# Optimization experiments

Measured on AMD Instinct MI355X. Metric: run time of the kernel, lower is better.

The kernel has to match this reference:

```python
import jax, jax.numpy as jnp
import numpy as np

NCONF, NT, NX = 8192, 64, 64


def setup_inputs() -> dict:
    key = jax.random.key(0)
    k1, k2, k3 = jax.random.split(key, 3)
    phi = jax.random.normal(k1, (NCONF, NT, NX), dtype=jnp.float32)
    # Well-conditioned invertible mixing matrix so logdet is finite/stable.
    W = jnp.eye(NX, dtype=jnp.float32) + 0.1 * jax.random.normal(k2, (NX, NX), dtype=jnp.float32)
    b = 0.1 * jax.random.normal(k3, (NX,), dtype=jnp.float32)
    return {"phi": phi, "W": W, "b": b}


def _nn(phi, W, b):
    # Wrapped NN: invertible linear coupling along the Nx axis.
    NNphi = jnp.einsum('btx,xy->bty', phi, W) + b
    _, logabsdet = jnp.linalg.slogdet(W)
    logDet = jnp.full((phi.shape[0],), phi.shape[1] * logabsdet, dtype=phi.dtype)
    return NNphi, logDet


def reference(phi, W, b):
    Nconf, Nt, Nx = phi.shape
    # t[i, x] = argmin over time of |phi[i, :, x]|  -> [Nconf, Nx]
    t = jnp.argmin(jnp.abs(phi), axis=1)
    # Source: if t[i,0] > t[i,1]: T0[i] = t[i,1]; config.flip(1) is DISCARDED (no-op).
    T0 = jnp.where(t[:, 0] > t[:, 1], t[:, 1], t[:, 0])  # [Nconf]
    j = jnp.arange(Nx)
    # torch.roll(x, s, dim): out[j] = x[(j - s) % N]
    idx_fwd = (j[None, :] - T0[:, None]) % Nx          # [Nconf, Nx]
    phi_r = jnp.take_along_axis(phi, idx_fwd[:, None, :], axis=2)
    NNphi, logDet = _nn(phi_r, W, b)
    # roll back with shift -T0; flip again discarded in source.
    idx_bwd = (j[None, :] + T0[:, None]) % Nx
    NNphi = jnp.take_along_axis(NNphi, idx_bwd[:, None, :], axis=2)
    return NNphi, logDet
```

## Files before the change

### kernel.cpp

```cpp
#include <hip/hip_runtime.h>
#include <stdint.h>


typedef _Float16 half2v __attribute__((ext_vector_type(2)));
typedef _Float16 half8v __attribute__((ext_vector_type(8)));
typedef float float4v __attribute__((ext_vector_type(4)));

#if defined(__has_builtin)
#if __has_builtin(__builtin_amdgcn_fdot2)
#define HAVE_FDOT2 1
#endif
#endif

__device__ __forceinline__ float dot2f(half2v a, half2v b, float c) {
#ifdef HAVE_FDOT2
  return __builtin_amdgcn_fdot2(a, b, c, false);
#else
  return c + (float)a.x * (float)b.x + (float)a.y * (float)b.y;
#endif
}

union H8 {
  half8v v;
  half2v p[4];
};

__global__ __launch_bounds__(64) void equiv_kernel(
    const float* __restrict__ phi, const float* __restrict__ W,
    const float* __restrict__ b, float* __restrict__ out) {
  __shared__ float smemF[4096];
  _Float16* sPhi = (_Float16*)smemF;
  _Float16* sW = ((_Float16*)smemF) + 4096;
  const int lane = threadIdx.x;

  if (blockIdx.x == 0) {
    float* A = smemF;
    for (int r = 0; r < 64; ++r) A[r * 64 + lane] = W[r * 64 + lane];
    __syncthreads();
    float ldsum = 0.f;
    for (int k = 0; k < 64; ++k) {
      __syncthreads();
      unsigned long long key = 0ull;
      if (lane >= k) {
        float v = fabsf(A[lane * 64 + k]);
        key = (((unsigned long long)__float_as_uint(v)) << 6) | (unsigned long long)lane;
      }
#pragma unroll
      for (int m = 1; m < 64; m <<= 1) {
        unsigned long long o = __shfl_xor(key, m);
        key = (o > key) ? o : key;
      }
      int p = (int)(key & 63ull);
      if (p != k) {
        float tk = A[k * 64 + lane], tp = A[p * 64 + lane];
        A[k * 64 + lane] = tp;
        A[p * 64 + lane] = tk;
      }
      __syncthreads();
      float akk = A[k * 64 + k];
      ldsum += logf(fabsf(akk));
      float rk = 1.0f / akk;
      float pivrow = A[k * 64 + lane];
      for (int t = k + 1; t < 64; ++t) {
        float m = A[t * 64 + k] * rk;
        if (lane > k) A[t * 64 + lane] -= m * pivrow;
      }
    }
    float ld = 64.0f * ldsum;
    float* outLD = out + (size_t)8192 * 4096;
    for (int it = 0; it < 128; ++it) outLD[it * 64 + lane] = ld;
    return;
  }

  const int cfg = (int)blockIdx.x - 1;
  const float4v* phiv = (const float4v*)(phi + (size_t)cfg * 4096);
  const float4v* Wv = (const float4v*)W;

  float4v pv[16], wv[16];
#pragma unroll
  for (int it = 0; it < 16; ++it) pv[it] = phiv[it * 64 + lane];
#pragma unroll
  for (int it = 0; it < 16; ++it) wv[it] = Wv[it * 64 + lane];

  unsigned long long k0 = ~0ull, k1 = ~0ull;
  if ((lane & 15) == 0) {
#pragma unroll
    for (int it = 0; it < 16; ++it) {
      int t = it * 4 + (lane >> 4);
      unsigned long long c0 =
          (((unsigned long long)__float_as_uint(fabsf(pv[it].x))) << 6) | (unsigned long long)t;
      unsigned long long c1 =
          (((unsigned long long)__float_as_uint(fabsf(pv[it].y))) << 6) | (unsigned long long)t;
      k0 = c0 < k0 ? c0 : k0;
      k1 = c1 < k1 ? c1 : k1;
    }
  }
#pragma unroll
  for (int m = 1; m < 64; m <<= 1) {
    unsigned long long o0 = __shfl_xor(k0, m);
    unsigned long long o1 = __shfl_xor(k1, m);
    k0 = o0 < k0 ? o0 : k0;
    k1 = o1 < k1 ? o1 : k1;
  }
  int t0i = (int)(k0 & 63ull), t1i = (int)(k1 & 63ull);
  int T0 = (t0i > t1i) ? t1i : t0i;

#pragma unroll
  for (int it = 0; it < 16; ++it) {
    int flat4 = it * 64 + lane;
    int t = flat4 >> 4;
    int xg = (flat4 & 15) << 2;
    int tsw = t >> 3;
#pragma unroll
    for (int kk = 0; kk < 4; ++kk) {
      int xp = (xg + kk + T0) & 63;
      int pos = t * 64 + ((((xp >> 3) ^ tsw) << 3) | (xp & 7));
      sPhi[pos] = (_Float16)pv[it][kk];
    }
  }
#pragma unroll
  for (int it = 0; it < 16; ++it) {
    int flat4 = it * 64 + lane;
    int xp = flat4 >> 4;
    int cg = (flat4 & 15) << 2;
#pragma unroll
    for (int kk = 0; kk < 4; ++kk) {
      int j = (cg + kk + 64 - T0) & 63;
      int pos = j * 64 + ((((xp >> 3) ^ (j >> 3)) << 3) | (xp & 7));
      sW[pos] = (_Float16)wv[it][kk];
    }
  }
  __syncthreads();

  const int ty = lane >> 3, tx = lane & 7;
  const int t0 = ty << 3, j0 = tx << 3;
  float acc[8][8];
#pragma unroll
  for (int r = 0; r < 8; ++r)
#pragma unroll
    for (int c = 0; c < 8; ++c) acc[r][c] = 0.f;

  for (int xb = 0; xb < 8; ++xb) {
    H8 a[8];
#pragma unroll
    for (int r = 0; r < 8; ++r)
      a[r].v = *(const half8v*)&sPhi[(t0 + r) * 64 + ((xb ^ ty) << 3)];
#pragma unroll
    for (int c = 0; c < 8; ++c) {
      H8 bb;
      bb.v = *(const half8v*)&sW[(j0 + c) * 64 + ((xb ^ tx) << 3)];
#pragma unroll
      for (int r = 0; r < 8; ++r) {
        float av = acc[r][c];
#pragma unroll
        for (int p = 0; p < 4; ++p) av = dot2f(a[r].p[p], bb.p[p], av);
        acc[r][c] = av;
      }
    }
  }

  float bv[8];
#pragma unroll
  for (int c = 0; c < 8; ++c) bv[c] = b[(j0 + c + T0) & 63];
  float* outp = out + (size_t)cfg * 4096;
#pragma unroll
  for (int r = 0; r < 8; ++r) {
#pragma unroll
    for (int cq = 0; cq < 2; ++cq) {
      float4v o;
#pragma unroll
      for (int kk = 0; kk < 4; ++kk) o[kk] = acc[r][cq * 4 + kk] + bv[cq * 4 + kk];
      *(float4v*)&outp[(t0 + r) * 64 + j0 + (cq << 2)] = o;
    }
  }
}

extern "C" void kernel_launch(void* const* d_in, const int* in_sizes, int n_in,
                              void* d_out, int out_size, void* d_ws, size_t ws_size,
                              hipStream_t stream) {
  const float* phi = (const float*)d_in[0];
  const float* W = (const float*)d_in[1];
  const float* b = (const float*)d_in[2];
  float* out = (float*)d_out;
  equiv_kernel<<<dim3(8193), dim3(64), 0, stream>>>(phi, W, b, out);
}
```

Baseline: 289.7 us.

## Precompute shifted fp16 W copies and pack four configs per block

Rolling phi by T0 is folded into the weights. A prep kernel writes all 64 doubly-shifted fp16 copies of W into workspace, and the main kernel reads the copy for its T0 straight from global memory/cache instead of scattering W into LDS for every configuration. Phi is now stored to LDS unshifted, using vectorized half4 stores. Each 256-thread block handles four configurations, one per wave, and the determinant path drops its barriers and uses a padded LDS layout. In exchange the inner GEMM loop now takes its B operand from global/L1, which may add latency, and there is an extra kernel launch plus a 512KB workspace.

```diff
diff --git a/kernel.cpp b/kernel.cpp
--- a/kernel.cpp
+++ b/kernel.cpp
@@ -3,6 +3,7 @@
 
 
 typedef _Float16 half2v __attribute__((ext_vector_type(2)));
+typedef _Float16 half4v __attribute__((ext_vector_type(4)));
 typedef _Float16 half8v __attribute__((ext_vector_type(8)));
 typedef float float4v __attribute__((ext_vector_type(4)));
 
@@ -25,26 +26,39 @@
   half2v p[4];
 };
 
-__global__ __launch_bounds__(64) void equiv_kernel(
+__global__ __launch_bounds__(256) void wt2_prep(const float* __restrict__ W,
+                                                _Float16* __restrict__ wt2) {
+  const int s = blockIdx.x;
+  const int tid = threadIdx.x;
+#pragma unroll
+  for (int it = 0; it < 16; ++it) {
+    int flat = it * 256 + tid;
+    int j = flat >> 6;
+    int y = flat & 63;
+    float v = W[((y + s) & 63) * 64 + ((j + s) & 63)];
+    wt2[(size_t)s * 4096 + flat] = (_Float16)v;
+  }
+}
+
+__global__ __launch_bounds__(256) void equiv_main(
     const float* __restrict__ phi, const float* __restrict__ W,
-    const float* __restrict__ b, float* __restrict__ out) {
-  __shared__ float smemF[4096];
-  _Float16* sPhi = (_Float16*)smemF;
-  _Float16* sW = ((_Float16*)smemF) + 4096;
-  const int lane = threadIdx.x;
+    const float* __restrict__ b, const _Float16* __restrict__ wt2,
+    float* __restrict__ out) {
+  __shared__ __align__(16) unsigned char smem[32768];
+  const int lane = threadIdx.x & 63;
 
   if (blockIdx.x == 0) {
-    float* A = smemF;
-    for (int r = 0; r < 64; ++r) A[r * 64 + lane] = W[r * 64 + lane];
-    __syncthreads();
+    if (threadIdx.x >= 64) return;
+    float* A = (float*)smem;
+    const int t = lane;
+    for (int r = 0; r < 64; ++r) A[r * 65 + lane] = W[r * 64 + lane];
     float ldsum = 0.f;
     for (int k = 0; k < 64; ++k) {
-      __syncthreads();
-      unsigned long long key = 0ull;
-      if (lane >= k) {
-        float v = fabsf(A[lane * 64 + k]);
-        key = (((unsigned long long)__float_as_uint(v)) << 6) | (unsigned long long)lane;
-      }
+      float av = (t >= k) ? fabsf(A[t * 65 + k]) : -1.0f;
+      unsigned long long key =
+          (((unsigned long long)__float_as_uint(av < 0.f ? 0.f : av)) << 6) |
+          (unsigned long long)t;
+      if (t < k) key = 0ull;
 #pragma unroll
       for (int m = 1; m < 64; m <<= 1) {
         unsigned long long o = __shfl_xor(key, m);
@@ -52,18 +66,18 @@
       }
       int p = (int)(key & 63ull);
       if (p != k) {
-        float tk = A[k * 64 + lane], tp = A[p * 64 + lane];
-        A[k * 64 + lane] = tp;
-        A[p * 64 + lane] = tk;
+        float vk = A[k * 65 + lane];
+        float vp = A[p * 65 + lane];
+        A[k * 65 + lane] = vp;
+        A[p * 65 + lane] = vk;
       }
-      __syncthreads();
-      float akk = A[k * 64 + k];
-      ldsum += logf(fabsf(akk));
-      float rk = 1.0f / akk;
-      float pivrow = A[k * 64 + lane];
-      for (int t = k + 1; t < 64; ++t) {
-        float m = A[t * 64 + k] * rk;
-        if (lane > k) A[t * 64 + lane] -= m * pivrow;
+      float piv = A[k * 65 + k];
+      ldsum += logf(fabsf(piv));
+      float rk = 1.0f / piv;
+      float m = (t > k) ? A[t * 65 + k] * rk : 0.f;
+      for (int c = k + 1; c < 64; ++c) {
+        float pr = A[k * 65 + c];
+        if (t > k) A[t * 65 + c] -= m * pr;
       }
     }
     float ld = 64.0f * ldsum;
@@ -72,25 +86,24 @@
     return;
   }
 
-  const int cfg = (int)blockIdx.x - 1;
+  const int wave = threadIdx.x >> 6;
+  const int cfg = ((int)blockIdx.x - 1) * 4 + wave;
+  _Float16* sPhi = ((_Float16*)smem) + wave * 4096;
+
   const float4v* phiv = (const float4v*)(phi + (size_t)cfg * 4096);
-  const float4v* Wv = (const float4v*)W;
-
-  float4v pv[16], wv[16];
+  float4v pv[16];
 #pragma unroll
   for (int it = 0; it < 16; ++it) pv[it] = phiv[it * 64 + lane];
-#pragma unroll
-  for (int it = 0; it < 16; ++it) wv[it] = Wv[it * 64 + lane];
 
   unsigned long long k0 = ~0ull, k1 = ~0ull;
   if ((lane & 15) == 0) {
 #pragma unroll
     for (int it = 0; it < 16; ++it) {
-      int t = it * 4 + (lane >> 4);
+      int tt = it * 4 + (lane >> 4);
       unsigned long long c0 =
-          (((unsigned long long)__float_as_uint(fabsf(pv[it].x))) << 6) | (unsigned long long)t;
+          (((unsigned long long)__float_as_uint(fabsf(pv[it].x))) << 6) | (unsigned long long)tt;
       unsigned long long c1 =
-          (((unsigned long long)__float_as_uint(fabsf(pv[it].y))) << 6) | (unsigned long long)t;
+          (((unsigned long long)__float_as_uint(fabsf(pv[it].y))) << 6) | (unsigned long long)tt;
       k0 = c0 < k0 ? c0 : k0;
       k1 = c1 < k1 ? c1 : k1;
     }
@@ -103,37 +116,26 @@
     k1 = o1 < k1 ? o1 : k1;
   }
   int t0i = (int)(k0 & 63ull), t1i = (int)(k1 & 63ull);
-  int T0 = (t0i > t1i) ? t1i : t0i;
+  const int T0 = (t0i > t1i) ? t1i : t0i;
 
 #pragma unroll
   for (int it = 0; it < 16; ++it) {
     int flat4 = it * 64 + lane;
     int t = flat4 >> 4;
-    int xg = (flat4 & 15) << 2;
-    int tsw = t >> 3;
-#pragma unroll
-    for (int kk = 0; kk < 4; ++kk) {
-      int xp = (xg + kk + T0) & 63;
-      int pos = t * 64 + ((((xp >> 3) ^ tsw) << 3) | (xp & 7));
-      sPhi[pos] = (_Float16)pv[it][kk];
-    }
+    int y0 = (flat4 & 15) << 2;
+    int ch = (y0 >> 3) ^ (t >> 3);
+    int off = y0 & 7;
+    half4v h;
+    h.x = (_Float16)pv[it].x;
+    h.y = (_Float16)pv[it].y;
+    h.z = (_Float16)pv[it].z;
+    h.w = (_Float16)pv[it].w;
+    *(half4v*)&sPhi[t * 64 + (ch << 3) + off] = h;
   }
-#pragma unroll
-  for (int it = 0; it < 16; ++it) {
-    int flat4 = it * 64 + lane;
-    int xp = flat4 >> 4;
-    int cg = (flat4 & 15) << 2;
-#pragma unroll
-    for (int kk = 0; kk < 4; ++kk) {
-      int j = (cg + kk + 64 - T0) & 63;
-      int pos = j * 64 + ((((xp >> 3) ^ (j >> 3)) << 3) | (xp & 7));
-      sW[pos] = (_Float16)wv[it][kk];
-    }
-  }
-  __syncthreads();
 
   const int ty = lane >> 3, tx = lane & 7;
   const int t0 = ty << 3, j0 = tx << 3;
+  const _Float16* wt = wt2 + (size_t)T0 * 4096;
   float acc[8][8];
 #pragma unroll
   for (int r = 0; r < 8; ++r)
@@ -148,7 +150,7 @@
 #pragma unroll
     for (int c = 0; c < 8; ++c) {
       H8 bb;
-      bb.v = *(const half8v*)&sW[(j0 + c) * 64 + ((xb ^ tx) << 3)];
+      bb.v = *(const half8v*)&wt[(j0 + c) * 64 + (xb << 3)];
 #pragma unroll
       for (int r = 0; r < 8; ++r) {
         float av = acc[r][c];
@@ -182,5 +184,8 @@
   const float* W = (const float*)d_in[1];
   const float* b = (const float*)d_in[2];
   float* out = (float*)d_out;
-  equiv_kernel<<<dim3(8193), dim3(64), 0, stream>>>(phi, W, b, out);
+  _Float16* wt2 = (_Float16*)d_ws;
+
+  wt2_prep<<<dim3(64), dim3(256), 0, stream>>>(W, wt2);
+  equiv_main<<<dim3(2049), dim3(256), 0, stream>>>(phi, W, b, wt2, out);
 }
```

After: 286.3 us. About the same (-1.2%).
